# Kernel tuning notes

Measured on AMD Instinct MI355X. Metric: run time of the kernel, lower is better.

Reference implementation:

```python
import jax, jax.numpy as jnp
import numpy as np

N_NODES = 50000
N_EDGES = 600000
NODE_DIM = 128
HIDDEN = 128
LN_EPS = 1e-5


def setup_inputs() -> dict:
    key = jax.random.key(0)
    ks = jax.random.split(key, 12)
    x = jax.random.normal(ks[0], (N_NODES, NODE_DIM), dtype=jnp.float32)
    edge_index = jax.random.randint(ks[1], (2, N_EDGES), 0, N_NODES, dtype=jnp.int32)
    # GCNConv weights (glorot-ish scaling)
    W1 = jax.random.normal(ks[2], (NODE_DIM, HIDDEN), dtype=jnp.float32) / np.sqrt(NODE_DIM)
    b1 = jnp.zeros((HIDDEN,), jnp.float32)
    W2 = jax.random.normal(ks[3], (HIDDEN, HIDDEN), dtype=jnp.float32) / np.sqrt(HIDDEN)
    b2 = jnp.zeros((HIDDEN,), jnp.float32)
    g1 = jnp.ones((HIDDEN,), jnp.float32)
    beta1 = jnp.zeros((HIDDEN,), jnp.float32)
    g2 = jnp.ones((HIDDEN,), jnp.float32)
    beta2 = jnp.zeros((HIDDEN,), jnp.float32)
    return {"x": x, "edge_index": edge_index, "W1": W1, "b1": b1, "g1": g1,
            "beta1": beta1, "W2": W2, "b2": b2, "g2": g2, "beta2": beta2}


def _gcn_conv(x, src, dst, norm, W, b, n):
    # x' = sum_{j->i} norm_ji * (x_j @ W) + b   (self-loops already in src/dst)
    h = x @ W                                   # [N, H]
    msg = h[src] * norm[:, None]                # [E+N, H]
    out = jax.ops.segment_sum(msg, dst, num_segments=n)
    return out + b


def _layer_norm(x, gamma, beta):
    mu = jnp.mean(x, axis=-1, keepdims=True)
    var = jnp.mean((x - mu) ** 2, axis=-1, keepdims=True)
    return (x - mu) * jax.lax.rsqrt(var + LN_EPS) * gamma + beta


def reference(x, edge_index, W1, b1, g1, beta1, W2, b2, g2, beta2):
    n = x.shape[0]
    loop = jnp.arange(n, dtype=edge_index.dtype)
    src = jnp.concatenate([edge_index[0], loop])
    dst = jnp.concatenate([edge_index[1], loop])
    # symmetric normalization with self-loops (PyG GCNConv default)
    deg = jax.ops.segment_sum(jnp.ones_like(dst, dtype=x.dtype), dst, num_segments=n)
    dinv = jnp.where(deg > 0, jax.lax.rsqrt(jnp.maximum(deg, 1.0)), 0.0)
    norm = dinv[src] * dinv[dst]                # [E+N]

    h = _gcn_conv(x, src, dst, norm, W1, b1, n)
    h = _layer_norm(h, g1, beta1)
    h = jax.nn.relu(h)                          # relu between layers only
    h = _gcn_conv(h, src, dst, norm, W2, b2, n)
    h = _layer_norm(h, g2, beta2)
    return h
```

## Files before the change

kernel.cpp:

```cpp
#include <hip/hip_runtime.h>

#define DIM 128
#define LN_EPS 1e-5f

typedef __attribute__((ext_vector_type(8))) short bf16x8;
typedef __attribute__((ext_vector_type(4))) float f32x4;

static __device__ __forceinline__ unsigned short f2bf(float f) {
    unsigned int u = __builtin_bit_cast(unsigned int, f);
    u += 0x7fffu + ((u >> 16) & 1u);
    return (unsigned short)(u >> 16);
}
static __device__ __forceinline__ float bf2f_lo(unsigned int u) {
    return __builtin_bit_cast(float, u << 16);
}
static __device__ __forceinline__ float bf2f_hi(unsigned int u) {
    return __builtin_bit_cast(float, u & 0xffff0000u);
}

__global__ __launch_bounds__(256) void wt_count_kernel(const float* __restrict__ W1,
                                                       const float* __restrict__ W2,
                                                       unsigned short* __restrict__ Wt1,
                                                       unsigned short* __restrict__ Wt2,
                                                       const int* __restrict__ dst,
                                                       int* __restrict__ counts,
                                                       int* __restrict__ rank, int E) {
    int b = blockIdx.x;
    if (b < 128) {
        int elem = b * 256 + threadIdx.x;
        int which = elem >> 14;
        int rest = elem & 16383;
        int c = rest >> 7;
        int k = rest & 127;
        const float* W = which ? W2 : W1;
        unsigned short* Wt = which ? Wt2 : Wt1;
        Wt[c * 128 + k] = f2bf(W[k * 128 + c]);
    } else {
        int e = (b - 128) * 256 + threadIdx.x;
        if (e < E) {
            int r = atomicAdd(&counts[dst[e]], 1);
            rank[e] = r;
        }
    }
}

__global__ __launch_bounds__(256) void scan_fused_kernel(const int* __restrict__ counts,
                                                         int* __restrict__ bsums,
                                                         int* __restrict__ bpref,
                                                         int* __restrict__ sync2,
                                                         int* __restrict__ rowptr,
                                                         float* __restrict__ dinv,
                                                         int n, int E, int nb) {
    __shared__ int ts[256];
    int tid = threadIdx.x;
    int b = blockIdx.x;
    int base = b * 1024 + tid * 4;
    int v[4];
#pragma unroll
    for (int j = 0; j < 4; ++j) {
        int i = base + j;
        v[j] = (i < n) ? counts[i] : 0;
        if (i < n) dinv[i] = rsqrtf((float)(v[j] + 1));
    }
    int s = v[0] + v[1] + v[2] + v[3];
    ts[tid] = s;
    __syncthreads();
    for (int off = 1; off < 256; off <<= 1) {
        int t2 = (tid >= off) ? ts[tid - off] : 0;
        __syncthreads();
        ts[tid] += t2;
        __syncthreads();
    }
    int excl = ts[tid] - s;

    if (tid == 255) {
        bsums[b] = ts[255];
        __threadfence();
        int t = atomicAdd(&sync2[0], 1);
        if (t == nb - 1) {
            __threadfence();
            int acc = 0;
            for (int k = 0; k < nb; ++k) {
                int sv = bsums[k];
                bpref[k] = acc;
                acc += sv;
            }
            __threadfence();
            atomicExch(&sync2[1], 1);
        }
    }
    if (tid == 0) {
        while (atomicAdd(&sync2[1], 0) == 0) { __builtin_amdgcn_s_sleep(8); }
    }
    __syncthreads();
    __threadfence();

    int pre = bpref[b] + excl;
#pragma unroll
    for (int j = 0; j < 4; ++j) {
        int i = base + j;
        if (i < n) rowptr[i] = pre;
        pre += v[j];
    }
    if (b == 0 && tid == 0) rowptr[n] = E;
}

__global__ __launch_bounds__(256) void gemm1_fill_kernel(const float* __restrict__ A,
                                                         const unsigned short* __restrict__ Bt,
                                                         const float* __restrict__ dinv,
                                                         unsigned short* __restrict__ H,
                                                         int n, int ntiles, int gG,
                                                         const int* __restrict__ src,
                                                         const int* __restrict__ dst,
                                                         const int* __restrict__ rowptr,
                                                         const int* __restrict__ rank,
                                                         unsigned short* __restrict__ colsrc,
                                                         int E) {
    __shared__ unsigned short Wlds[128 * 136];
    if (blockIdx.x >= gG) {
        int e = (blockIdx.x - gG) * 256 + threadIdx.x;
        if (e < E) {
            int p = rowptr[dst[e]] + rank[e];
            colsrc[p] = (unsigned short)src[e];
        }
        return;
    }
    for (int u = threadIdx.x; u < 2048; u += 256) {
        int row = u >> 4;
        int sub = u & 15;
        *(bf16x8*)&Wlds[row * 136 + sub * 8] = *(const bf16x8*)(Bt + row * 128 + sub * 8);
    }
    __syncthreads();

    int wid = threadIdx.x >> 6;
    int lane = threadIdx.x & 63;
    int tile = blockIdx.x * 4 + wid;
    if (tile >= ntiles) tile = ntiles - 1;
    int r0 = tile * 16;
    int mrow = lane & 15;
    int kgrp = lane >> 4;

    int arow_i = r0 + mrow;
    if (arow_i > n - 1) arow_i = n - 1;
    const float* arow = A + (size_t)arow_i * DIM + kgrp * 8;

    f32x4 acc[8];
#pragma unroll
    for (int t = 0; t < 8; ++t) acc[t] = (f32x4){0.f, 0.f, 0.f, 0.f};

#pragma unroll
    for (int kc = 0; kc < 4; ++kc) {
        float4 v0 = *(const float4*)(arow + kc * 32);
        float4 v1 = *(const float4*)(arow + kc * 32 + 4);
        bf16x8 af;
        af[0] = (short)f2bf(v0.x); af[1] = (short)f2bf(v0.y);
        af[2] = (short)f2bf(v0.z); af[3] = (short)f2bf(v0.w);
        af[4] = (short)f2bf(v1.x); af[5] = (short)f2bf(v1.y);
        af[6] = (short)f2bf(v1.z); af[7] = (short)f2bf(v1.w);
#pragma unroll
        for (int t = 0; t < 8; ++t) {
            bf16x8 bfv = *(const bf16x8*)&Wlds[(t * 16 + mrow) * 136 + kc * 32 + kgrp * 8];
            acc[t] = __builtin_amdgcn_mfma_f32_16x16x32_bf16(af, bfv, acc[t], 0, 0, 0);
        }
    }

    float dv[4];
#pragma unroll
    for (int reg = 0; reg < 4; ++reg) {
        int rr = r0 + kgrp * 4 + reg;
        dv[reg] = (rr < n) ? dinv[rr] : 0.f;
    }

    __syncthreads();

    unsigned short* Wst = &Wlds[wid * 16 * 136];
#pragma unroll
    for (int t = 0; t < 8; ++t) {
#pragma unroll
        for (int reg = 0; reg < 4; ++reg) {
            Wst[(kgrp * 4 + reg) * 136 + t * 16 + mrow] = f2bf(acc[t][reg] * dv[reg]);
        }
    }

#pragma unroll
    for (int q = 0; q < 4; ++q) {
        int e = q * 64 + lane;
        int row = e >> 4;
        int c16 = e & 15;
        int grow = r0 + row;
        if (grow < n) {
            *(bf16x8*)&H[(size_t)grow * DIM + c16 * 8] = *(const bf16x8*)&Wst[row * 136 + c16 * 8];
        }
    }
}

__global__ __launch_bounds__(128, 5) void gather_gemm_kernel(const int* __restrict__ rowptr,
                                                             const unsigned short* __restrict__ colsrc,
                                                             const uint4* __restrict__ H4,
                                                             const float* __restrict__ dinv,
                                                             const float* __restrict__ bias,
                                                             const float* __restrict__ gamma,
                                                             const float* __restrict__ beta,
                                                             const unsigned short* __restrict__ Wt2,
                                                             unsigned short* __restrict__ H2,
                                                             int n) {
    __shared__ unsigned short Tl[16][136];
    int wid = threadIdx.x >> 6;
    int lane = threadIdx.x & 63;
    int r0 = blockIdx.x * 16;
    int grp = lane >> 4;
    int gl = lane & 15;

#pragma unroll
    for (int t = 0; t < 2; ++t) {
        int r = r0 + wid * 8 + t * 4 + grp;
        int rc = (r < n) ? r : (n - 1);
        float di = dinv[rc];
        uint4 su = H4[(size_t)rc * 16 + gl];
        int p0 = rowptr[rc];
        int p1 = rowptr[rc + 1];
        float a0 = bf2f_lo(su.x), a1 = bf2f_hi(su.x);
        float a2 = bf2f_lo(su.y), a3 = bf2f_hi(su.y);
        float a4 = bf2f_lo(su.z), a5 = bf2f_hi(su.z);
        float a6 = bf2f_lo(su.w), a7 = bf2f_hi(su.w);

        int deg = p1 - p0;
        int m = max(deg, __shfl_xor(deg, 16));
        m = max(m, __shfl_xor(m, 32));
        int nch = (m + 15) >> 4;

        for (int c = 0; c < nch; ++c) {
            int cb = c * 16;
            int gi = p0 + cb + gl;
            gi = gi < p1 ? gi : p1 - 1;
            int idxv = (int)colsrc[gi];

            uint4 h[16];
#pragma unroll
            for (int j = 0; j < 16; ++j) {
                int sS = __shfl(idxv, grp * 16 + j);
                h[j] = H4[(size_t)sS * 16 + gl];
            }
#pragma unroll
            for (int j = 0; j < 16; ++j) {
                bool act = (cb + j < deg);
                a0 += act ? bf2f_lo(h[j].x) : 0.f;
                a1 += act ? bf2f_hi(h[j].x) : 0.f;
                a2 += act ? bf2f_lo(h[j].y) : 0.f;
                a3 += act ? bf2f_hi(h[j].y) : 0.f;
                a4 += act ? bf2f_lo(h[j].z) : 0.f;
                a5 += act ? bf2f_hi(h[j].z) : 0.f;
                a6 += act ? bf2f_lo(h[j].w) : 0.f;
                a7 += act ? bf2f_hi(h[j].w) : 0.f;
            }
        }

        float4 bb0 = ((const float4*)bias)[gl * 2];
        float4 bb1 = ((const float4*)bias)[gl * 2 + 1];
        float v0 = a0 * di + bb0.x;
        float v1 = a1 * di + bb0.y;
        float v2 = a2 * di + bb0.z;
        float v3 = a3 * di + bb0.w;
        float v4 = a4 * di + bb1.x;
        float v5 = a5 * di + bb1.y;
        float v6 = a6 * di + bb1.z;
        float v7 = a7 * di + bb1.w;

        float s1 = v0 + v1 + v2 + v3 + v4 + v5 + v6 + v7;
        float s2 = v0 * v0 + v1 * v1 + v2 * v2 + v3 * v3 +
                   v4 * v4 + v5 * v5 + v6 * v6 + v7 * v7;
#pragma unroll
        for (int off = 8; off > 0; off >>= 1) {
            s1 += __shfl_xor(s1, off);
            s2 += __shfl_xor(s2, off);
        }
        float mu = s1 * (1.f / 128.f);
        float var = s2 * (1.f / 128.f) - mu * mu;
        float rstd = rsqrtf(var + LN_EPS);

        float4 gg0 = ((const float4*)gamma)[gl * 2];
        float4 gg1 = ((const float4*)gamma)[gl * 2 + 1];
        float4 be0 = ((const float4*)beta)[gl * 2];
        float4 be1 = ((const float4*)beta)[gl * 2 + 1];

        float o0 = fmaxf((v0 - mu) * rstd * gg0.x + be0.x, 0.f);
        float o1 = fmaxf((v1 - mu) * rstd * gg0.y + be0.y, 0.f);
        float o2 = fmaxf((v2 - mu) * rstd * gg0.z + be0.z, 0.f);
        float o3 = fmaxf((v3 - mu) * rstd * gg0.w + be0.w, 0.f);
        float o4 = fmaxf((v4 - mu) * rstd * gg1.x + be1.x, 0.f);
        float o5 = fmaxf((v5 - mu) * rstd * gg1.y + be1.y, 0.f);
        float o6 = fmaxf((v6 - mu) * rstd * gg1.z + be1.z, 0.f);
        float o7 = fmaxf((v7 - mu) * rstd * gg1.w + be1.w, 0.f);

        bf16x8 pk;
        pk[0] = (short)f2bf(o0); pk[1] = (short)f2bf(o1);
        pk[2] = (short)f2bf(o2); pk[3] = (short)f2bf(o3);
        pk[4] = (short)f2bf(o4); pk[5] = (short)f2bf(o5);
        pk[6] = (short)f2bf(o6); pk[7] = (short)f2bf(o7);
        *(bf16x8*)&Tl[wid * 8 + t * 4 + grp][gl * 8] = pk;
    }

    __syncthreads();

    int mrow = lane & 15;
    int kg = lane >> 4;
    f32x4 acc[4];
#pragma unroll
    for (int tt = 0; tt < 4; ++tt) acc[tt] = (f32x4){0.f, 0.f, 0.f, 0.f};

#pragma unroll
    for (int kc = 0; kc < 4; ++kc) {
        bf16x8 af = *(const bf16x8*)&Tl[mrow][kc * 32 + kg * 8];
#pragma unroll
        for (int tt = 0; tt < 4; ++tt) {
            int trow = (wid * 4 + tt) * 16 + mrow;
            bf16x8 bv = *(const bf16x8*)(Wt2 + (size_t)trow * 128 + kc * 32 + kg * 8);
            acc[tt] = __builtin_amdgcn_mfma_f32_16x16x32_bf16(af, bv, acc[tt], 0, 0, 0);
        }
    }

    float dv[4];
#pragma unroll
    for (int reg = 0; reg < 4; ++reg) {
        int rr = r0 + kg * 4 + reg;
        dv[reg] = (rr < n) ? dinv[rr] : 0.f;
    }

    __syncthreads();

#pragma unroll
    for (int tt = 0; tt < 4; ++tt) {
#pragma unroll
        for (int reg = 0; reg < 4; ++reg) {
            Tl[kg * 4 + reg][(wid * 4 + tt) * 16 + mrow] = f2bf(acc[tt][reg] * dv[reg]);
        }
    }
    __syncthreads();

#pragma unroll
    for (int q = 0; q < 2; ++q) {
        int e = q * 128 + threadIdx.x;
        int row = e >> 4;
        int c16 = e & 15;
        int grow = r0 + row;
        if (grow < n) {
            *(bf16x8*)&H2[(size_t)grow * DIM + c16 * 8] = *(const bf16x8*)&Tl[row][c16 * 8];
        }
    }
}

__global__ __launch_bounds__(256, 5) void gather_out_kernel(const int* __restrict__ rowptr,
                                                            const unsigned short* __restrict__ colsrc,
                                                            const uint4* __restrict__ H4,
                                                            const float* __restrict__ dinv,
                                                            const float* __restrict__ bias,
                                                            const float* __restrict__ gamma,
                                                            const float* __restrict__ beta,
                                                            float* __restrict__ out,
                                                            int n) {
    int wid = threadIdx.x >> 6;
    int lane = threadIdx.x & 63;
    int grp = lane >> 4;
    int gl = lane & 15;
    int r = blockIdx.x * 16 + wid * 4 + grp;
    int valid = (r < n);
    int rc = valid ? r : (n - 1);

    float di = dinv[rc];
    uint4 su = H4[(size_t)rc * 16 + gl];
    int p0 = rowptr[rc];
    int p1 = rowptr[rc + 1];
    float a0 = bf2f_lo(su.x), a1 = bf2f_hi(su.x);
    float a2 = bf2f_lo(su.y), a3 = bf2f_hi(su.y);
    float a4 = bf2f_lo(su.z), a5 = bf2f_hi(su.z);
    float a6 = bf2f_lo(su.w), a7 = bf2f_hi(su.w);

    int deg = p1 - p0;
    int m = max(deg, __shfl_xor(deg, 16));
    m = max(m, __shfl_xor(m, 32));
    int nch = (m + 15) >> 4;

    for (int c = 0; c < nch; ++c) {
        int cb = c * 16;
        int gi = p0 + cb + gl;
        gi = gi < p1 ? gi : p1 - 1;
        int idxv = (int)colsrc[gi];

        uint4 h[16];
#pragma unroll
        for (int j = 0; j < 16; ++j) {
            int sS = __shfl(idxv, grp * 16 + j);
            h[j] = H4[(size_t)sS * 16 + gl];
        }
#pragma unroll
        for (int j = 0; j < 16; ++j) {
            bool act = (cb + j < deg);
            a0 += act ? bf2f_lo(h[j].x) : 0.f;
            a1 += act ? bf2f_hi(h[j].x) : 0.f;
            a2 += act ? bf2f_lo(h[j].y) : 0.f;
            a3 += act ? bf2f_hi(h[j].y) : 0.f;
            a4 += act ? bf2f_lo(h[j].z) : 0.f;
            a5 += act ? bf2f_hi(h[j].z) : 0.f;
            a6 += act ? bf2f_lo(h[j].w) : 0.f;
            a7 += act ? bf2f_hi(h[j].w) : 0.f;
        }
    }

    float4 bb0 = ((const float4*)bias)[gl * 2];
    float4 bb1 = ((const float4*)bias)[gl * 2 + 1];
    float v0 = a0 * di + bb0.x;
    float v1 = a1 * di + bb0.y;
    float v2 = a2 * di + bb0.z;
    float v3 = a3 * di + bb0.w;
    float v4 = a4 * di + bb1.x;
    float v5 = a5 * di + bb1.y;
    float v6 = a6 * di + bb1.z;
    float v7 = a7 * di + bb1.w;

    float s1 = v0 + v1 + v2 + v3 + v4 + v5 + v6 + v7;
    float s2 = v0 * v0 + v1 * v1 + v2 * v2 + v3 * v3 +
               v4 * v4 + v5 * v5 + v6 * v6 + v7 * v7;
#pragma unroll
    for (int off = 8; off > 0; off >>= 1) {
        s1 += __shfl_xor(s1, off);
        s2 += __shfl_xor(s2, off);
    }
    float mu = s1 * (1.f / 128.f);
    float var = s2 * (1.f / 128.f) - mu * mu;
    float rstd = rsqrtf(var + LN_EPS);

    float4 gg0 = ((const float4*)gamma)[gl * 2];
    float4 gg1 = ((const float4*)gamma)[gl * 2 + 1];
    float4 be0 = ((const float4*)beta)[gl * 2];
    float4 be1 = ((const float4*)beta)[gl * 2 + 1];

    float o0 = (v0 - mu) * rstd * gg0.x + be0.x;
    float o1 = (v1 - mu) * rstd * gg0.y + be0.y;
    float o2 = (v2 - mu) * rstd * gg0.z + be0.z;
    float o3 = (v3 - mu) * rstd * gg0.w + be0.w;
    float o4 = (v4 - mu) * rstd * gg1.x + be1.x;
    float o5 = (v5 - mu) * rstd * gg1.y + be1.y;
    float o6 = (v6 - mu) * rstd * gg1.z + be1.z;
    float o7 = (v7 - mu) * rstd * gg1.w + be1.w;

    if (valid) {
        ((float4*)out)[(size_t)r * 32 + gl * 2] = make_float4(o0, o1, o2, o3);
        ((float4*)out)[(size_t)r * 32 + gl * 2 + 1] = make_float4(o4, o5, o6, o7);
    }
}

extern "C" void kernel_launch(void* const* d_in, const int* in_sizes, int n_in,
                              void* d_out, int out_size, void* d_ws, size_t ws_size,
                              hipStream_t stream) {
    const float* x   = (const float*)d_in[0];
    const int*   ei  = (const int*)d_in[1];
    const float* W1  = (const float*)d_in[2];
    const float* b1  = (const float*)d_in[3];
    const float* g1  = (const float*)d_in[4];
    const float* be1 = (const float*)d_in[5];
    const float* W2  = (const float*)d_in[6];
    const float* b2  = (const float*)d_in[7];
    const float* g2  = (const float*)d_in[8];
    const float* be2 = (const float*)d_in[9];

    int n = in_sizes[0] / DIM;
    int E = in_sizes[1] / 2;
    const int* src = ei;
    const int* dst = ei + E;

    char* wp = (char*)d_ws;
    auto alloc = [&](size_t bytes) {
        void* p = (void*)wp;
        wp += (bytes + 255) & ~(size_t)255;
        return p;
    };
    float*          dinv   = (float*)alloc((size_t)n * 4);
    int*            counts = (int*)alloc((size_t)(n + 64) * 4);
    int*            sync2  = counts + n;
    int*            rowptr = (int*)alloc((size_t)(n + 1) * 4);
    int*            rank   = (int*)alloc((size_t)E * 4);
    int*            bsums  = (int*)alloc(256 * 4);
    int*            bpref  = (int*)alloc(256 * 4);
    unsigned short* colsrc = (unsigned short*)alloc((size_t)E * 2);
    unsigned short* Wt1    = (unsigned short*)alloc(128 * 128 * 2);
    unsigned short* Wt2    = (unsigned short*)alloc(128 * 128 * 2);
    unsigned short* H      = (unsigned short*)alloc((size_t)n * DIM * 2);
    unsigned short* H2     = (unsigned short*)alloc((size_t)n * DIM * 2);

    hipMemsetAsync(counts, 0, (size_t)(n + 64) * 4, stream);

    int gE = (E + 255) / 256;
    wt_count_kernel<<<128 + gE, 256, 0, stream>>>(W1, W2, Wt1, Wt2, dst, counts, rank, E);

    int nb1 = (n + 1023) / 1024;
    scan_fused_kernel<<<nb1, 256, 0, stream>>>(counts, bsums, bpref, sync2,
                                               rowptr, dinv, n, E, nb1);

    int ntiles = (n + 15) / 16;
    int gG = (ntiles + 3) / 4;

    gemm1_fill_kernel<<<gG + gE, 256, 0, stream>>>(x, Wt1, dinv, H, n, ntiles, gG,
                                                   src, dst, rowptr, rank, colsrc, E);

    gather_gemm_kernel<<<ntiles, 128, 0, stream>>>(rowptr, colsrc, (const uint4*)H, dinv,
                                                   b1, g1, be1, Wt2, H2, n);

    gather_out_kernel<<<ntiles, 256, 0, stream>>>(rowptr, colsrc, (const uint4*)H2, dinv,
                                                  b2, g2, be2, (float*)d_out, n);
}
```

Measured before the change: 217.1 us.

## Split feature matrix into column slices and gather per slice

Result: slower. 235.0 us (+8.3%).

```diff
diff --git a/kernel.cpp b/kernel.cpp
--- a/kernel.cpp
+++ b/kernel.cpp
@@ -108,7 +108,7 @@
 __global__ __launch_bounds__(256) void gemm1_fill_kernel(const float* __restrict__ A,
                                                          const unsigned short* __restrict__ Bt,
                                                          const float* __restrict__ dinv,
-                                                         unsigned short* __restrict__ H,
+                                                         unsigned short* __restrict__ Hs,
                                                          int n, int ntiles, int gG,
                                                          const int* __restrict__ src,
                                                          const int* __restrict__ dst,
@@ -185,25 +185,74 @@
 #pragma unroll
     for (int q = 0; q < 4; ++q) {
         int e = q * 64 + lane;
-        int row = e >> 4;
-        int c16 = e & 15;
-        int grow = r0 + row;
+        int s = e >> 5;
+        int node = (e >> 1) & 15;
+        int half = e & 1;
+        int grow = r0 + node;
         if (grow < n) {
-            *(bf16x8*)&H[(size_t)grow * DIM + c16 * 8] = *(const bf16x8*)&Wst[row * 136 + c16 * 8];
-        }
-    }
-}
-
-__global__ __launch_bounds__(128, 5) void gather_gemm_kernel(const int* __restrict__ rowptr,
-                                                             const unsigned short* __restrict__ colsrc,
-                                                             const uint4* __restrict__ H4,
-                                                             const float* __restrict__ dinv,
-                                                             const float* __restrict__ bias,
-                                                             const float* __restrict__ gamma,
-                                                             const float* __restrict__ beta,
-                                                             const unsigned short* __restrict__ Wt2,
-                                                             unsigned short* __restrict__ H2,
-                                                             int n) {
+            *(bf16x8*)&Hs[((size_t)s * n + grow) * 16 + half * 8] =
+                *(const bf16x8*)&Wst[node * 136 + s * 16 + half * 8];
+        }
+    }
+}
+
+__global__ __launch_bounds__(256) void slice_gather_kernel(const int* __restrict__ rowptr,
+                                                           const unsigned short* __restrict__ colsrc,
+                                                           const unsigned short* __restrict__ Tb,
+                                                           float* __restrict__ S,
+                                                           int n) {
+    int s = blockIdx.x & 7;
+    int g = blockIdx.x >> 3;
+    int lane = threadIdx.x & 63;
+    int wid = threadIdx.x >> 6;
+    int sub = lane >> 3;
+    int sl = lane & 7;
+    int r = g * 32 + wid * 8 + sub;
+    int rc = (r < n) ? r : (n - 1);
+    int p0 = rowptr[rc];
+    int p1 = rowptr[rc + 1];
+    int deg = p1 - p0;
+    int m = deg;
+    m = max(m, __shfl_xor(m, 1));
+    m = max(m, __shfl_xor(m, 2));
+    m = max(m, __shfl_xor(m, 4));
+    int nch = (m + 7) >> 3;
+    const unsigned short* Ts = Tb + (size_t)s * n * 16;
+    int lbase = lane & ~7;
+    float c0 = 0.f, c1 = 0.f;
+
+    for (int c = 0; c < nch; ++c) {
+        int cb = c * 8;
+        int gi = p0 + cb + sl;
+        gi = gi < p1 ? gi : p1 - 1;
+        int idxv = (int)colsrc[gi];
+#pragma unroll
+        for (int j = 0; j < 8; ++j) {
+            int sidx = __shfl(idxv, lbase + j);
+            unsigned int v = *(const unsigned int*)(Ts + (size_t)sidx * 16 + sl * 2);
+            bool act = (cb + j < deg);
+            c0 += act ? bf2f_lo(v) : 0.f;
+            c1 += act ? bf2f_hi(v) : 0.f;
+        }
+    }
+
+    if (r < n) {
+        float2 st = make_float2(c0, c1);
+        __builtin_nontemporal_store(
+            __builtin_bit_cast(unsigned long long, st),
+            (unsigned long long*)(S + ((size_t)s * n + r) * 16 + sl * 2));
+    }
+}
+
+__global__ __launch_bounds__(128, 5) void ln_gemm_kernel(const float* __restrict__ S,
+                                                         const unsigned short* __restrict__ Hs,
+                                                         const float* __restrict__ dinv,
+                                                         const float* __restrict__ bias,
+                                                         const float* __restrict__ gamma,
+                                                         const float* __restrict__ beta,
+                                                         const unsigned short* __restrict__ Wt2,
+                                                         unsigned short* __restrict__ H2s,
+                                                         int n) {
     __shared__ unsigned short Tl[16][136];
     int wid = threadIdx.x >> 6;
     int lane = threadIdx.x & 63;
@@ -211,52 +260,28 @@
     int grp = lane >> 4;
     int gl = lane & 15;
 
+    float4 bb0 = ((const float4*)bias)[gl * 2];
+    float4 bb1 = ((const float4*)bias)[gl * 2 + 1];
+    float4 gg0 = ((const float4*)gamma)[gl * 2];
+    float4 gg1 = ((const float4*)gamma)[gl * 2 + 1];
+    float4 be0 = ((const float4*)beta)[gl * 2];
+    float4 be1 = ((const float4*)beta)[gl * 2 + 1];
+
 #pragma unroll
     for (int t = 0; t < 2; ++t) {
         int r = r0 + wid * 8 + t * 4 + grp;
         int rc = (r < n) ? r : (n - 1);
         float di = dinv[rc];
-        uint4 su = H4[(size_t)rc * 16 + gl];
-        int p0 = rowptr[rc];
-        int p1 = rowptr[rc + 1];
-        float a0 = bf2f_lo(su.x), a1 = bf2f_hi(su.x);
-        float a2 = bf2f_lo(su.y), a3 = bf2f_hi(su.y);
-        float a4 = bf2f_lo(su.z), a5 = bf2f_hi(su.z);
-        float a6 = bf2f_lo(su.w), a7 = bf2f_hi(su.w);
-
-        int deg = p1 - p0;
-        int m = max(deg, __shfl_xor(deg, 16));
-        m = max(m, __shfl_xor(m, 32));
-        int nch = (m + 15) >> 4;
-
-        for (int c = 0; c < nch; ++c) {
-            int cb = c * 16;
-            int gi = p0 + cb + gl;
-            gi = gi < p1 ? gi : p1 - 1;
-            int idxv = (int)colsrc[gi];
-
-            uint4 h[16];
-#pragma unroll
-            for (int j = 0; j < 16; ++j) {
-                int sS = __shfl(idxv, grp * 16 + j);
-                h[j] = H4[(size_t)sS * 16 + gl];
-            }
-#pragma unroll
-            for (int j = 0; j < 16; ++j) {
-                bool act = (cb + j < deg);
-                a0 += act ? bf2f_lo(h[j].x) : 0.f;
-                a1 += act ? bf2f_hi(h[j].x) : 0.f;
-                a2 += act ? bf2f_lo(h[j].y) : 0.f;
-                a3 += act ? bf2f_hi(h[j].y) : 0.f;
-                a4 += act ? bf2f_lo(h[j].z) : 0.f;
-                a5 += act ? bf2f_hi(h[j].z) : 0.f;
-                a6 += act ? bf2f_lo(h[j].w) : 0.f;
-                a7 += act ? bf2f_hi(h[j].w) : 0.f;
-            }
-        }
-
-        float4 bb0 = ((const float4*)bias)[gl * 2];
-        float4 bb1 = ((const float4*)bias)[gl * 2 + 1];
+        size_t off = ((size_t)(gl >> 1) * n + rc) * 16 + (gl & 1) * 8;
+        uint4 su = *(const uint4*)(Hs + off);
+        float4 s0 = *(const float4*)(S + off);
+        float4 s1 = *(const float4*)(S + off + 4);
+
+        float a0 = bf2f_lo(su.x) + s0.x, a1 = bf2f_hi(su.x) + s0.y;
+        float a2 = bf2f_lo(su.y) + s0.z, a3 = bf2f_hi(su.y) + s0.w;
+        float a4 = bf2f_lo(su.z) + s1.x, a5 = bf2f_hi(su.z) + s1.y;
+        float a6 = bf2f_lo(su.w) + s1.z, a7 = bf2f_hi(su.w) + s1.w;
+
         float v0 = a0 * di + bb0.x;
         float v1 = a1 * di + bb0.y;
         float v2 = a2 * di + bb0.z;
@@ -266,22 +291,17 @@
         float v6 = a6 * di + bb1.z;
         float v7 = a7 * di + bb1.w;
 
-        float s1 = v0 + v1 + v2 + v3 + v4 + v5 + v6 + v7;
-        float s2 = v0 * v0 + v1 * v1 + v2 * v2 + v3 * v3 +
-                   v4 * v4 + v5 * v5 + v6 * v6 + v7 * v7;
-#pragma unroll
-        for (int off = 8; off > 0; off >>= 1) {
-            s1 += __shfl_xor(s1, off);
-            s2 += __shfl_xor(s2, off);
-        }
-        float mu = s1 * (1.f / 128.f);
-        float var = s2 * (1.f / 128.f) - mu * mu;
+        float s1r = v0 + v1 + v2 + v3 + v4 + v5 + v6 + v7;
+        float s2r = v0 * v0 + v1 * v1 + v2 * v2 + v3 * v3 +
+                    v4 * v4 + v5 * v5 + v6 * v6 + v7 * v7;
+#pragma unroll
+        for (int off2 = 8; off2 > 0; off2 >>= 1) {
+            s1r += __shfl_xor(s1r, off2);
+            s2r += __shfl_xor(s2r, off2);
+        }
+        float mu = s1r * (1.f / 128.f);
+        float var = s2r * (1.f / 128.f) - mu * mu;
         float rstd = rsqrtf(var + LN_EPS);
-
-        float4 gg0 = ((const float4*)gamma)[gl * 2];
-        float4 gg1 = ((const float4*)gamma)[gl * 2 + 1];
-        float4 be0 = ((const float4*)beta)[gl * 2];
-        float4 be1 = ((const float4*)beta)[gl * 2 + 1];
 
         float o0 = fmaxf((v0 - mu) * rstd * gg0.x + be0.x, 0.f);
         float o1 = fmaxf((v1 - mu) * rstd * gg0.y + be0.y, 0.f);
@@ -340,24 +360,25 @@
 #pragma unroll
     for (int q = 0; q < 2; ++q) {
         int e = q * 128 + threadIdx.x;
-        int row = e >> 4;
-        int c16 = e & 15;
-        int grow = r0 + row;
+        int s = e >> 5;
+        int node = (e >> 1) & 15;
+        int half = e & 1;
+        int grow = r0 + node;
         if (grow < n) {
-            *(bf16x8*)&H2[(size_t)grow * DIM + c16 * 8] = *(const bf16x8*)&Tl[row][c16 * 8];
-        }
-    }
-}
-
-__global__ __launch_bounds__(256, 5) void gather_out_kernel(const int* __restrict__ rowptr,
-                                                            const unsigned short* __restrict__ colsrc,
-                                                            const uint4* __restrict__ H4,
-                                                            const float* __restrict__ dinv,
-                                                            const float* __restrict__ bias,
-                                                            const float* __restrict__ gamma,
-                                                            const float* __restrict__ beta,
-                                                            float* __restrict__ out,
-                                                            int n) {
+            *(bf16x8*)&H2s[((size_t)s * n + grow) * 16 + half * 8] =
+                *(const bf16x8*)&Tl[node][s * 16 + half * 8];
+        }
+    }
+}
+
+__global__ __launch_bounds__(256, 5) void ln_out_kernel(const float* __restrict__ S,
+                                                        const unsigned short* __restrict__ Hs,
+                                                        const float* __restrict__ dinv,
+                                                        const float* __restrict__ bias,
+                                                        const float* __restrict__ gamma,
+                                                        const float* __restrict__ beta,
+                                                        float* __restrict__ out,
+                                                        int n) {
     int wid = threadIdx.x >> 6;
     int lane = threadIdx.x & 63;
     int grp = lane >> 4;
@@ -367,44 +388,15 @@
     int rc = valid ? r : (n - 1);
 
     float di = dinv[rc];
-    uint4 su = H4[(size_t)rc * 16 + gl];
-    int p0 = rowptr[rc];
-    int p1 = rowptr[rc + 1];
-    float a0 = bf2f_lo(su.x), a1 = bf2f_hi(su.x);
-    float a2 = bf2f_lo(su.y), a3 = bf2f_hi(su.y);
-    float a4 = bf2f_lo(su.z), a5 = bf2f_hi(su.z);
-    float a6 = bf2f_lo(su.w), a7 = bf2f_hi(su.w);
-
-    int deg = p1 - p0;
-    int m = max(deg, __shfl_xor(deg, 16));
-    m = max(m, __shfl_xor(m, 32));
-    int nch = (m + 15) >> 4;
-
-    for (int c = 0; c < nch; ++c) {
-        int cb = c * 16;
-        int gi = p0 + cb + gl;
-        gi = gi < p1 ? gi : p1 - 1;
-        int idxv = (int)colsrc[gi];
-
-        uint4 h[16];
-#pragma unroll
-        for (int j = 0; j < 16; ++j) {
-            int sS = __shfl(idxv, grp * 16 + j);
-            h[j] = H4[(size_t)sS * 16 + gl];
-        }
-#pragma unroll
-        for (int j = 0; j < 16; ++j) {
-            bool act = (cb + j < deg);
-            a0 += act ? bf2f_lo(h[j].x) : 0.f;
-            a1 += act ? bf2f_hi(h[j].x) : 0.f;
-            a2 += act ? bf2f_lo(h[j].y) : 0.f;
-            a3 += act ? bf2f_hi(h[j].y) : 0.f;
-            a4 += act ? bf2f_lo(h[j].z) : 0.f;
-            a5 += act ? bf2f_hi(h[j].z) : 0.f;
-            a6 += act ? bf2f_lo(h[j].w) : 0.f;
-            a7 += act ? bf2f_hi(h[j].w) : 0.f;
-        }
-    }
+    size_t off = ((size_t)(gl >> 1) * n + rc) * 16 + (gl & 1) * 8;
+    uint4 su = *(const uint4*)(Hs + off);
+    float4 s0 = *(const float4*)(S + off);
+    float4 s1 = *(const float4*)(S + off + 4);
+
+    float a0 = bf2f_lo(su.x) + s0.x, a1 = bf2f_hi(su.x) + s0.y;
+    float a2 = bf2f_lo(su.y) + s0.z, a3 = bf2f_hi(su.y) + s0.w;
+    float a4 = bf2f_lo(su.z) + s1.x, a5 = bf2f_hi(su.z) + s1.y;
+    float a6 = bf2f_lo(su.w) + s1.z, a7 = bf2f_hi(su.w) + s1.w;
 
     float4 bb0 = ((const float4*)bias)[gl * 2];
     float4 bb1 = ((const float4*)bias)[gl * 2 + 1];
@@ -417,16 +409,16 @@
     float v6 = a6 * di + bb1.z;
     float v7 = a7 * di + bb1.w;
 
-    float s1 = v0 + v1 + v2 + v3 + v4 + v5 + v6 + v7;
-    float s2 = v0 * v0 + v1 * v1 + v2 * v2 + v3 * v3 +
-               v4 * v4 + v5 * v5 + v6 * v6 + v7 * v7;
-#pragma unroll
-    for (int off = 8; off > 0; off >>= 1) {
-        s1 += __shfl_xor(s1, off);
-        s2 += __shfl_xor(s2, off);
-    }
-    float mu = s1 * (1.f / 128.f);
-    float var = s2 * (1.f / 128.f) - mu * mu;
+    float s1r = v0 + v1 + v2 + v3 + v4 + v5 + v6 + v7;
+    float s2r = v0 * v0 + v1 * v1 + v2 * v2 + v3 * v3 +
+                v4 * v4 + v5 * v5 + v6 * v6 + v7 * v7;
+#pragma unroll
+    for (int off2 = 8; off2 > 0; off2 >>= 1) {
+        s1r += __shfl_xor(s1r, off2);
+        s2r += __shfl_xor(s2r, off2);
+    }
+    float mu = s1r * (1.f / 128.f);
+    float var = s2r * (1.f / 128.f) - mu * mu;
     float rstd = rsqrtf(var + LN_EPS);
 
     float4 gg0 = ((const float4*)gamma)[gl * 2];
@@ -484,8 +476,9 @@
     unsigned short* colsrc = (unsigned short*)alloc((size_t)E * 2);
     unsigned short* Wt1    = (unsigned short*)alloc(128 * 128 * 2);
     unsigned short* Wt2    = (unsigned short*)alloc(128 * 128 * 2);
-    unsigned short* H      = (unsigned short*)alloc((size_t)n * DIM * 2);
-    unsigned short* H2     = (unsigned short*)alloc((size_t)n * DIM * 2);
+    unsigned short* Hs     = (unsigned short*)alloc((size_t)n * DIM * 2);
+    unsigned short* H2s    = (unsigned short*)alloc((size_t)n * DIM * 2);
+    float*          S      = (float*)alloc((size_t)n * DIM * 4);
 
     hipMemsetAsync(counts, 0, (size_t)(n + 64) * 4, stream);
 
@@ -498,13 +491,14 @@
 
     int ntiles = (n + 15) / 16;
     int gG = (ntiles + 3) / 4;
-
-    gemm1_fill_kernel<<<gG + gE, 256, 0, stream>>>(x, Wt1, dinv, H, n, ntiles, gG,
+    int ngrp = (n + 31) / 32;
+
+    gemm1_fill_kernel<<<gG + gE, 256, 0, stream>>>(x, Wt1, dinv, Hs, n, ntiles, gG,
                                                    src, dst, rowptr, rank, colsrc, E);
 
-    gather_gemm_kernel<<<ntiles, 128, 0, stream>>>(rowptr, colsrc, (const uint4*)H, dinv,
-                                                   b1, g1, be1, Wt2, H2, n);
-
-    gather_out_kernel<<<ntiles, 256, 0, stream>>>(rowptr, colsrc, (const uint4*)H2, dinv,
-                                                  b2, g2, be2, (float*)d_out, n);
-}
+    slice_gather_kernel<<<ngrp * 8, 256, 0, stream>>>(rowptr, colsrc, Hs, S, n);
+    ln_gemm_kernel<<<ntiles, 128, 0, stream>>>(S, Hs, dinv, b1, g1, be1, Wt2, H2s, n);
+
+    slice_gather_kernel<<<ngrp * 8, 256, 0, stream>>>(rowptr, colsrc, H2s, S, n);
+    ln_out_kernel<<<ntiles, 256, 0, stream>>>(S, H2s, dinv, b2, g2, be2, (float*)d_out, n);
+}
```
